# Performance work log

Measured on AMD Instinct MI355X. Metric: run time of the kernel, lower is better.

The kernel has to match this reference:

```python
import jax, jax.numpy as jnp
import numpy as np

B, S1, S2, H1, H2, HID = 8, 512, 512, 128, 128, 128

def setup_inputs() -> dict:
    key = jax.random.key(0)
    ks = jax.random.split(key, 8)
    return {
        "query": jax.random.normal(ks[0], (B, S1, H1), jnp.float32),
        "key": jax.random.normal(ks[1], (B, S2, H2), jnp.float32),
        "value": jax.random.normal(ks[2], (B, S2, H2), jnp.float32),
        "q_mask": jax.random.randint(ks[3], (B, S1), 0, 2, jnp.int32),
        "k_mask": jax.random.randint(ks[4], (B, S2), 0, 2, jnp.int32),
        # init_weights: Linear weight ~ N(0, 0.01), bias = 0
        "W1": jax.random.normal(ks[5], (HID, H1 + H2), jnp.float32) * 0.01,
        "b1": jnp.zeros((HID,), jnp.float32),
        "W2": jax.random.normal(ks[6], (1, HID), jnp.float32) * 0.01,
        "b2": jnp.zeros((1,), jnp.float32),
    }

def reference(query, key, value, q_mask, k_mask, W1, b1, W2, b2):
    h1 = query.shape[-1]
    # Linear on concat([q,k]) == q @ W1[:, :h1].T + k @ W1[:, h1:].T + b1
    qp = jnp.einsum('bsd,hd->bsh', query, W1[:, :h1]) + b1   # [B,S1,HID]
    kp = jnp.einsum('btd,hd->bth', key, W1[:, h1:])          # [B,S2,HID]
    h = jax.nn.relu(qp[:, :, None, :] + kp[:, None, :, :])   # [B,S1,S2,HID]
    s = jnp.einsum('bsth,h->bst', h, W2[0]) + b2[0]          # [B,S1,S2]
    mask = (q_mask[:, :, None] * k_mask[:, None, :]) > 0     # [B,S1,S2]
    A = jnp.where(mask, jnp.exp(s), 0.0)                     # masked_fill(-inf).exp()
    A_sum = jnp.clip(jnp.sum(A, axis=-1, keepdims=True), 2e-15, None)
    attn = A / A_sum
    return jnp.einsum('bst,btd->bsd', attn, value)           # [B,S1,H2]
```

## Files before the change

### kernel.cpp

```cpp
#include <hip/hip_runtime.h>

#define S 512
#define H 128
#define NROW 4096
#define TI 8

__global__ __launch_bounds__(256) void proj_kernel(
    const float* __restrict__ query, const float* __restrict__ key,
    const float* __restrict__ W1, const float* __restrict__ b1,
    float* __restrict__ qp, float* __restrict__ kp)
{
  __shared__ float w1t[128][130];
  const int bid = blockIdx.x;
  const bool isq = bid < 128;
  const float* __restrict__ src = isq ? query : key;
  const int rbase = (isq ? bid : bid - 128) * 32;
  const int off = isq ? 0 : 128;
  const int tid = threadIdx.x;

  for (int idx = tid; idx < 128 * 32; idx += 256) {
    const int d4 = idx & 31, h = idx >> 5;
    const float4 v = *(const float4*)(W1 + h * 256 + off + d4 * 4);
    w1t[d4 * 4 + 0][h] = v.x;
    w1t[d4 * 4 + 1][h] = v.y;
    w1t[d4 * 4 + 2][h] = v.z;
    w1t[d4 * 4 + 3][h] = v.w;
  }
  __syncthreads();

  const int w = __builtin_amdgcn_readfirstlane(tid >> 6);
  const int lane = tid & 63;
  const int r0 = rbase + w * 8;

  float acc[8][2];
  float2 bv = make_float2(0.f, 0.f);
  if (isq) bv = *(const float2*)(b1 + 2 * lane);
  #pragma unroll
  for (int r = 0; r < 8; r++) { acc[r][0] = bv.x; acc[r][1] = bv.y; }

  for (int dc = 0; dc < 128; dc += 8) {
    float qs[8][8];
    #pragma unroll
    for (int r = 0; r < 8; r++) {
      const float* sp = src + (size_t)(r0 + r) * H + dc;
      #pragma unroll
      for (int u = 0; u < 8; u++) qs[r][u] = sp[u];
    }
    #pragma unroll
    for (int dd = 0; dd < 8; dd++) {
      const float2 wv = *(const float2*)&w1t[dc + dd][2 * lane];
      #pragma unroll
      for (int r = 0; r < 8; r++) {
        acc[r][0] = __builtin_fmaf(qs[r][dd], wv.x, acc[r][0]);
        acc[r][1] = __builtin_fmaf(qs[r][dd], wv.y, acc[r][1]);
      }
    }
  }
  float* __restrict__ dst = isq ? qp : kp;
  #pragma unroll
  for (int r = 0; r < 8; r++) {
    *(float2*)(dst + (size_t)(r0 + r) * H + 2 * lane) =
        make_float2(acc[r][0], acc[r][1]);
  }
}

__global__ __launch_bounds__(256) void attn_kernel(
    const float* __restrict__ qp, const float* __restrict__ kp,
    const float* __restrict__ value, const int* __restrict__ q_mask,
    const int* __restrict__ k_mask, const float* __restrict__ W2,
    const float* __restrict__ b2,
    float* __restrict__ nump, float* __restrict__ denp)
{
  __shared__ float aT[4][64][12];
  __shared__ float numk[TI][132];
  __shared__ float denk[TI];

  const int it = blockIdx.x;
  const int jh = blockIdx.y;
  const int r0 = it * TI;
  const int b  = r0 >> 9;
  const int tid = threadIdx.x;
  const int w = __builtin_amdgcn_readfirstlane(tid >> 6);
  const int lane = tid & 63;
  const int jl = (jh << 8) + (w << 6) + lane;
  const int jg = (b << 9) + jl;
  const int km = k_mask[jg];
  const float* __restrict__ kprow = kp + (size_t)jg * H;
  const float b2v = b2[0];

  float s[TI];
  #pragma unroll
  for (int i = 0; i < TI; i++) s[i] = 0.f;

  for (int hc = 0; hc < H; hc += 16) {
    float kr[16];
    #pragma unroll
    for (int u = 0; u < 4; u++) {
      const float4 v4 = *(const float4*)(kprow + hc + u * 4);
      kr[u*4+0] = v4.x; kr[u*4+1] = v4.y; kr[u*4+2] = v4.z; kr[u*4+3] = v4.w;
    }
    float w2r[16];
    #pragma unroll
    for (int u = 0; u < 16; u++) w2r[u] = W2[hc + u];
    #pragma unroll
    for (int i = 0; i < TI; i++) {
      const float* __restrict__ qrow = qp + (size_t)(r0 + i) * H + hc;
      #pragma unroll
      for (int u = 0; u < 16; u++) {
        float t = fmaxf(qrow[u] + kr[u], 0.f);
        s[i] = __builtin_fmaf(t, w2r[u], s[i]);
      }
    }
  }

  float a[TI], den[TI];
  #pragma unroll
  for (int i = 0; i < TI; i++) {
    const int qm = q_mask[r0 + i];
    a[i] = (km > 0 && qm > 0) ? __expf(s[i] + b2v) : 0.f;
  }
  #pragma unroll
  for (int i = 0; i < TI; i++) {
    float d = a[i];
    #pragma unroll
    for (int m = 32; m >= 1; m >>= 1) d += __shfl_xor(d, m, 64);
    den[i] = d;
  }
  #pragma unroll
  for (int i = 0; i < TI; i++) aT[w][lane][i] = a[i];
  __syncthreads();

  const int lj = lane >> 5, lh = lane & 31;
  float nr[TI][4];
  #pragma unroll
  for (int i = 0; i < TI; i++) { nr[i][0]=0.f; nr[i][1]=0.f; nr[i][2]=0.f; nr[i][3]=0.f; }
  const float* __restrict__ vbase =
      value + ((size_t)b * S + (jh << 8) + (w << 6)) * H;

  for (int js = 0; js < 32; js++) {
    const int j = js * 2 + lj;
    const float4 vv = *(const float4*)(vbase + (size_t)j * H + lh * 4);
    float av[TI];
    { const float4 t0 = *(const float4*)&aT[w][j][0];
      const float4 t1 = *(const float4*)&aT[w][j][4];
      av[0]=t0.x; av[1]=t0.y; av[2]=t0.z; av[3]=t0.w;
      av[4]=t1.x; av[5]=t1.y; av[6]=t1.z; av[7]=t1.w; }
    #pragma unroll
    for (int i = 0; i < TI; i++) {
      nr[i][0] = __builtin_fmaf(av[i], vv.x, nr[i][0]);
      nr[i][1] = __builtin_fmaf(av[i], vv.y, nr[i][1]);
      nr[i][2] = __builtin_fmaf(av[i], vv.z, nr[i][2]);
      nr[i][3] = __builtin_fmaf(av[i], vv.w, nr[i][3]);
    }
  }
  #pragma unroll
  for (int i = 0; i < TI; i++) {
    #pragma unroll
    for (int k = 0; k < 4; k++) nr[i][k] += __shfl_xor(nr[i][k], 32, 64);
  }

  for (int r = 0; r < 4; r++) {
    if (w == r) {
      if (lj == 0) {
        #pragma unroll
        for (int i = 0; i < TI; i++) {
          float4* p = (float4*)&numk[i][lh * 4];
          if (r == 0) {
            *p = make_float4(nr[i][0], nr[i][1], nr[i][2], nr[i][3]);
          } else {
            float4 t = *p;
            t.x += nr[i][0]; t.y += nr[i][1]; t.z += nr[i][2]; t.w += nr[i][3];
            *p = t;
          }
        }
      }
      if (lane == 0) {
        #pragma unroll
        for (int i = 0; i < TI; i++)
          denk[i] = (r == 0) ? den[i] : denk[i] + den[i];
      }
    }
    __syncthreads();
  }

  {
    const int i = tid >> 5, seg = tid & 31;
    const float4 v = *(const float4*)&numk[i][seg * 4];
    float* dst = nump + ((size_t)jh * NROW + (size_t)(r0 + i)) * H + seg * 4;
    *(float4*)dst = v;
    if (tid < TI) denp[jh * NROW + r0 + tid] = denk[tid];
  }
}

__global__ __launch_bounds__(256) void finalize_kernel(
    const float* __restrict__ nump, const float* __restrict__ denp,
    float* __restrict__ out)
{
  const int idx = blockIdx.x * 256 + threadIdx.x;
  const int row = idx >> 5;
  const float4 a = *(const float4*)(nump + (size_t)idx * 4);
  const float4 c = *(const float4*)(nump + (size_t)NROW * H + (size_t)idx * 4);
  const float d = denp[row] + denp[NROW + row];
  const float inv = 1.f / fmaxf(d, 2e-15f);
  float4 o;
  o.x = (a.x + c.x) * inv; o.y = (a.y + c.y) * inv;
  o.z = (a.z + c.z) * inv; o.w = (a.w + c.w) * inv;
  *(float4*)(out + (size_t)idx * 4) = o;
}

extern "C" void kernel_launch(void* const* d_in, const int* in_sizes, int n_in,
                              void* d_out, int out_size, void* d_ws, size_t ws_size,
                              hipStream_t stream)
{
  (void)in_sizes; (void)n_in; (void)out_size; (void)ws_size;
  const float* query  = (const float*)d_in[0];
  const float* key    = (const float*)d_in[1];
  const float* value  = (const float*)d_in[2];
  const int*   q_mask = (const int*)d_in[3];
  const int*   k_mask = (const int*)d_in[4];
  const float* W1     = (const float*)d_in[5];
  const float* b1     = (const float*)d_in[6];
  const float* W2     = (const float*)d_in[7];
  const float* b2     = (const float*)d_in[8];
  float* out = (float*)d_out;

  float* ws   = (float*)d_ws;
  float* qp   = ws;
  float* kp   = ws + (size_t)NROW * H;
  float* nump = ws + (size_t)2 * NROW * H;
  float* denp = ws + (size_t)4 * NROW * H;

  proj_kernel<<<256, 256, 0, stream>>>(query, key, W1, b1, qp, kp);
  attn_kernel<<<dim3(512, 2), 256, 0, stream>>>(qp, kp, value, q_mask, k_mask,
                                                W2, b2, nump, denp);
  finalize_kernel<<<512, 256, 0, stream>>>(nump, denp, out);
}
```

Measured before the change: 121.7 us.

## Rewrite relu as abs identity and transpose key projection for coalesced loads

Uses relu(x) = (x + |x|)/2 so the linear part of the score splits into per-row terms (qp·W2/2, kp·W2/2). These terms are precomputed in the projection kernel, leaving an fma on fabs in the inner loop. The key projection is written transposed so adjacent lanes read adjacent addresses, and query rows plus a halved W2 are staged in shared memory instead of being reread from global memory. Projection blocks are halved in size so twice as many are launched. The costs are an extra shuffle reduction, a shared-memory transpose in the projection kernel, and slightly different floating-point rounding.

Result: slower. 127.4 us (+4.8%).

```diff
diff --git a/kernel.cpp b/kernel.cpp
--- a/kernel.cpp
+++ b/kernel.cpp
@@ -8,13 +8,16 @@
 __global__ __launch_bounds__(256) void proj_kernel(
     const float* __restrict__ query, const float* __restrict__ key,
     const float* __restrict__ W1, const float* __restrict__ b1,
-    float* __restrict__ qp, float* __restrict__ kp)
+    const float* __restrict__ W2,
+    float* __restrict__ qp, float* __restrict__ kpT,
+    float* __restrict__ qw, float* __restrict__ kw)
 {
   __shared__ float w1t[128][130];
+  __shared__ float kt[16][132];
   const int bid = blockIdx.x;
-  const bool isq = bid < 128;
+  const bool isq = bid < 256;
   const float* __restrict__ src = isq ? query : key;
-  const int rbase = (isq ? bid : bid - 128) * 32;
+  const int rbase = (isq ? bid : bid - 256) * 16;
   const int off = isq ? 0 : 128;
   const int tid = threadIdx.x;
 
@@ -30,19 +33,19 @@
 
   const int w = __builtin_amdgcn_readfirstlane(tid >> 6);
   const int lane = tid & 63;
-  const int r0 = rbase + w * 8;
-
-  float acc[8][2];
+  const int r0w = rbase + w * 4;
+
+  float acc[4][2];
   float2 bv = make_float2(0.f, 0.f);
   if (isq) bv = *(const float2*)(b1 + 2 * lane);
   #pragma unroll
-  for (int r = 0; r < 8; r++) { acc[r][0] = bv.x; acc[r][1] = bv.y; }
+  for (int r = 0; r < 4; r++) { acc[r][0] = bv.x; acc[r][1] = bv.y; }
 
   for (int dc = 0; dc < 128; dc += 8) {
-    float qs[8][8];
-    #pragma unroll
-    for (int r = 0; r < 8; r++) {
-      const float* sp = src + (size_t)(r0 + r) * H + dc;
+    float qs[4][8];
+    #pragma unroll
+    for (int r = 0; r < 4; r++) {
+      const float* sp = src + (size_t)(r0w + r) * H + dc;
       #pragma unroll
       for (int u = 0; u < 8; u++) qs[r][u] = sp[u];
     }
@@ -50,27 +53,57 @@
     for (int dd = 0; dd < 8; dd++) {
       const float2 wv = *(const float2*)&w1t[dc + dd][2 * lane];
       #pragma unroll
-      for (int r = 0; r < 8; r++) {
+      for (int r = 0; r < 4; r++) {
         acc[r][0] = __builtin_fmaf(qs[r][dd], wv.x, acc[r][0]);
         acc[r][1] = __builtin_fmaf(qs[r][dd], wv.y, acc[r][1]);
       }
     }
   }
-  float* __restrict__ dst = isq ? qp : kp;
-  #pragma unroll
-  for (int r = 0; r < 8; r++) {
-    *(float2*)(dst + (size_t)(r0 + r) * H + 2 * lane) =
-        make_float2(acc[r][0], acc[r][1]);
+
+  const float2 w2p = *(const float2*)(W2 + 2 * lane);
+  #pragma unroll
+  for (int r = 0; r < 4; r++) {
+    float t = acc[r][0] * w2p.x + acc[r][1] * w2p.y;
+    #pragma unroll
+    for (int m = 1; m <= 32; m <<= 1) t += __shfl_xor(t, m, 64);
+    if (lane == 0) {
+      float* dw = isq ? qw : kw;
+      dw[r0w + r] = 0.5f * t;
+    }
+  }
+
+  if (isq) {
+    #pragma unroll
+    for (int r = 0; r < 4; r++)
+      *(float2*)(qp + (size_t)(r0w + r) * H + 2 * lane) =
+          make_float2(acc[r][0], acc[r][1]);
+  } else {
+    #pragma unroll
+    for (int r = 0; r < 4; r++)
+      *(float2*)&kt[w * 4 + r][2 * lane] =
+          make_float2(acc[r][0], acc[r][1]);
+    __syncthreads();
+    const int h = tid >> 1, seg = tid & 1;
+    float tmp[8];
+    #pragma unroll
+    for (int c = 0; c < 8; c++) tmp[c] = kt[seg * 8 + c][h];
+    float* dst = kpT + (size_t)h * NROW + rbase + seg * 8;
+    *(float4*)dst = make_float4(tmp[0], tmp[1], tmp[2], tmp[3]);
+    *(float4*)(dst + 4) = make_float4(tmp[4], tmp[5], tmp[6], tmp[7]);
   }
 }
 
 __global__ __launch_bounds__(256) void attn_kernel(
-    const float* __restrict__ qp, const float* __restrict__ kp,
+    const float* __restrict__ qp, const float* __restrict__ kpT,
+    const float* __restrict__ qw, const float* __restrict__ kw,
     const float* __restrict__ value, const int* __restrict__ q_mask,
     const int* __restrict__ k_mask, const float* __restrict__ W2,
     const float* __restrict__ b2,
     float* __restrict__ nump, float* __restrict__ denp)
 {
+  __shared__ float qs[TI][128];
+  __shared__ float w2s[128];
+  __shared__ float qws[TI];
   __shared__ float aT[4][64][12];
   __shared__ float numk[TI][132];
   __shared__ float denk[TI];
@@ -85,30 +118,48 @@
   const int jl = (jh << 8) + (w << 6) + lane;
   const int jg = (b << 9) + jl;
   const int km = k_mask[jg];
-  const float* __restrict__ kprow = kp + (size_t)jg * H;
+  const float kwj = kw[jg];
   const float b2v = b2[0];
 
+  {
+    const int i = tid >> 5, c = tid & 31;
+    *(float4*)&qs[i][c * 4] = *(const float4*)(qp + (size_t)(r0 + i) * H + c * 4);
+    if (tid < 32) {
+      float4 t = *(const float4*)(W2 + tid * 4);
+      t.x *= 0.5f; t.y *= 0.5f; t.z *= 0.5f; t.w *= 0.5f;
+      *(float4*)&w2s[tid * 4] = t;
+    }
+    if (tid < TI) qws[tid] = qw[r0 + tid];
+  }
+  __syncthreads();
+
   float s[TI];
   #pragma unroll
   for (int i = 0; i < TI; i++) s[i] = 0.f;
+  const float* __restrict__ kcol = kpT + jg;
 
   for (int hc = 0; hc < H; hc += 16) {
     float kr[16];
     #pragma unroll
+    for (int u = 0; u < 16; u++) kr[u] = kcol[(hc + u) * NROW];
+    float w2c[16];
+    #pragma unroll
     for (int u = 0; u < 4; u++) {
-      const float4 v4 = *(const float4*)(kprow + hc + u * 4);
-      kr[u*4+0] = v4.x; kr[u*4+1] = v4.y; kr[u*4+2] = v4.z; kr[u*4+3] = v4.w;
-    }
-    float w2r[16];
-    #pragma unroll
-    for (int u = 0; u < 16; u++) w2r[u] = W2[hc + u];
+      const float4 t = *(const float4*)&w2s[hc + u * 4];
+      w2c[u*4+0] = t.x; w2c[u*4+1] = t.y; w2c[u*4+2] = t.z; w2c[u*4+3] = t.w;
+    }
     #pragma unroll
     for (int i = 0; i < TI; i++) {
-      const float* __restrict__ qrow = qp + (size_t)(r0 + i) * H + hc;
+      float qv[16];
+      #pragma unroll
+      for (int u = 0; u < 4; u++) {
+        const float4 t = *(const float4*)&qs[i][hc + u * 4];
+        qv[u*4+0] = t.x; qv[u*4+1] = t.y; qv[u*4+2] = t.z; qv[u*4+3] = t.w;
+      }
       #pragma unroll
       for (int u = 0; u < 16; u++) {
-        float t = fmaxf(qrow[u] + kr[u], 0.f);
-        s[i] = __builtin_fmaf(t, w2r[u], s[i]);
+        const float t = qv[u] + kr[u];
+        s[i] = __builtin_fmaf(fabsf(t), w2c[u], s[i]);
       }
     }
   }
@@ -117,7 +168,8 @@
   #pragma unroll
   for (int i = 0; i < TI; i++) {
     const int qm = q_mask[r0 + i];
-    a[i] = (km > 0 && qm > 0) ? __expf(s[i] + b2v) : 0.f;
+    const float sf = s[i] + qws[i] + kwj;
+    a[i] = (km > 0 && qm > 0) ? __expf(sf + b2v) : 0.f;
   }
   #pragma unroll
   for (int i = 0; i < TI; i++) {
@@ -226,12 +278,14 @@
 
   float* ws   = (float*)d_ws;
   float* qp   = ws;
-  float* kp   = ws + (size_t)NROW * H;
-  float* nump = ws + (size_t)2 * NROW * H;
-  float* denp = ws + (size_t)4 * NROW * H;
-
-  proj_kernel<<<256, 256, 0, stream>>>(query, key, W1, b1, qp, kp);
-  attn_kernel<<<dim3(512, 2), 256, 0, stream>>>(qp, kp, value, q_mask, k_mask,
-                                                W2, b2, nump, denp);
+  float* kpT  = ws + (size_t)NROW * H;
+  float* qw   = ws + (size_t)2 * NROW * H;
+  float* kw   = qw + NROW;
+  float* nump = kw + NROW;
+  float* denp = nump + (size_t)2 * NROW * H;
+
+  proj_kernel<<<512, 256, 0, stream>>>(query, key, W1, b1, W2, qp, kpT, qw, kw);
+  attn_kernel<<<dim3(512, 2), 256, 0, stream>>>(qp, kpT, qw, kw, value, q_mask,
+                                                k_mask, W2, b2, nump, denp);
   finalize_kernel<<<512, 256, 0, stream>>>(nump, denp, out);
 }
```

## Use relu(x)=(x+|x|)/2 split, fuse finalize into attention, transpose W1 once

Applied to the files above, without the earlier changes.

Rewrites relu(q+k)·w2 as 0.5·(q·w2 + k·w2) + 0.5·|q+k|·w2. The linear parts are precomputed per row in the projection kernel, which trims the inner loop to an add, an abs and an FMA. The attention kernel now covers all 512 keys per block with 512 threads and writes normalized output directly, so the split-K partial buffers and the finalize kernel are gone. W1 is transposed once by a small kernel and read from global memory instead of being re-transposed into LDS per block. kp is stored in an h-blocked layout for coalesced per-key loads. This adds a kernel launch and changes the reduction order.

Result: slower. 128.6 us (+5.7%).

```diff
diff --git a/kernel.cpp b/kernel.cpp
--- a/kernel.cpp
+++ b/kernel.cpp
@@ -5,207 +5,221 @@
 #define NROW 4096
 #define TI 8
 
+__global__ __launch_bounds__(256) void w1t_kernel(const float* __restrict__ W1,
+                                                  float* __restrict__ w1T) {
+  __shared__ float t[32][33];
+  const int d0 = (blockIdx.x & 7) * 32;
+  const int h0 = (blockIdx.x >> 3) * 32;
+  const int tx = threadIdx.x & 31, ty = threadIdx.x >> 5;
+  #pragma unroll
+  for (int r = 0; r < 4; r++)
+    t[ty + r * 8][tx] = W1[(h0 + ty + r * 8) * 256 + d0 + tx];
+  __syncthreads();
+  #pragma unroll
+  for (int r = 0; r < 4; r++)
+    w1T[(size_t)(d0 + ty + r * 8) * H + h0 + tx] = t[tx][ty + r * 8];
+}
+
 __global__ __launch_bounds__(256) void proj_kernel(
     const float* __restrict__ query, const float* __restrict__ key,
-    const float* __restrict__ W1, const float* __restrict__ b1,
-    float* __restrict__ qp, float* __restrict__ kp)
+    const float* __restrict__ w1T, const float* __restrict__ b1,
+    const float* __restrict__ W2, const float* __restrict__ b2,
+    float* __restrict__ qp, float* __restrict__ kp2,
+    float* __restrict__ qw, float* __restrict__ kw)
 {
-  __shared__ float w1t[128][130];
   const int bid = blockIdx.x;
-  const bool isq = bid < 128;
+  const bool isq = bid < 256;
   const float* __restrict__ src = isq ? query : key;
-  const int rbase = (isq ? bid : bid - 128) * 32;
-  const int off = isq ? 0 : 128;
+  const int rbase = (isq ? bid : bid - 256) * 16;
+  const int doff = isq ? 0 : 128;
   const int tid = threadIdx.x;
-
-  for (int idx = tid; idx < 128 * 32; idx += 256) {
-    const int d4 = idx & 31, h = idx >> 5;
-    const float4 v = *(const float4*)(W1 + h * 256 + off + d4 * 4);
-    w1t[d4 * 4 + 0][h] = v.x;
-    w1t[d4 * 4 + 1][h] = v.y;
-    w1t[d4 * 4 + 2][h] = v.z;
-    w1t[d4 * 4 + 3][h] = v.w;
-  }
-  __syncthreads();
-
   const int w = __builtin_amdgcn_readfirstlane(tid >> 6);
   const int lane = tid & 63;
-  const int r0 = rbase + w * 8;
-
-  float acc[8][2];
+  const int r0w = rbase + w * 4;
+
+  float acc[4][2];
   float2 bv = make_float2(0.f, 0.f);
   if (isq) bv = *(const float2*)(b1 + 2 * lane);
   #pragma unroll
-  for (int r = 0; r < 8; r++) { acc[r][0] = bv.x; acc[r][1] = bv.y; }
+  for (int r = 0; r < 4; r++) { acc[r][0] = bv.x; acc[r][1] = bv.y; }
 
   for (int dc = 0; dc < 128; dc += 8) {
-    float qs[8][8];
-    #pragma unroll
-    for (int r = 0; r < 8; r++) {
-      const float* sp = src + (size_t)(r0 + r) * H + dc;
+    float qs[4][8];
+    #pragma unroll
+    for (int r = 0; r < 4; r++) {
+      const float* sp = src + (size_t)(r0w + r) * H + dc;
       #pragma unroll
       for (int u = 0; u < 8; u++) qs[r][u] = sp[u];
     }
     #pragma unroll
     for (int dd = 0; dd < 8; dd++) {
-      const float2 wv = *(const float2*)&w1t[dc + dd][2 * lane];
+      const float2 wv =
+          *(const float2*)(w1T + (size_t)(doff + dc + dd) * H + 2 * lane);
       #pragma unroll
-      for (int r = 0; r < 8; r++) {
+      for (int r = 0; r < 4; r++) {
         acc[r][0] = __builtin_fmaf(qs[r][dd], wv.x, acc[r][0]);
         acc[r][1] = __builtin_fmaf(qs[r][dd], wv.y, acc[r][1]);
       }
     }
   }
-  float* __restrict__ dst = isq ? qp : kp;
-  #pragma unroll
-  for (int r = 0; r < 8; r++) {
-    *(float2*)(dst + (size_t)(r0 + r) * H + 2 * lane) =
-        make_float2(acc[r][0], acc[r][1]);
-  }
-}
-
-__global__ __launch_bounds__(256) void attn_kernel(
-    const float* __restrict__ qp, const float* __restrict__ kp,
+
+  const float2 w2p = *(const float2*)(W2 + 2 * lane);
+  const float b2v = b2[0];
+  #pragma unroll
+  for (int r = 0; r < 4; r++) {
+    float t = acc[r][0] * w2p.x + acc[r][1] * w2p.y;
+    #pragma unroll
+    for (int m = 1; m <= 32; m <<= 1) t += __shfl_xor(t, m, 64);
+    if (lane == 0) {
+      if (isq) qw[r0w + r] = 0.5f * t + b2v;
+      else     kw[r0w + r] = 0.5f * t;
+    }
+  }
+
+  if (isq) {
+    #pragma unroll
+    for (int r = 0; r < 4; r++)
+      *(float2*)(qp + (size_t)(r0w + r) * H + 2 * lane) =
+          make_float2(acc[r][0], acc[r][1]);
+  } else {
+    #pragma unroll
+    for (int r = 0; r < 4; r++)
+      *(float2*)(kp2 + ((size_t)(lane >> 3) * NROW + (r0w + r)) * 16 +
+                 (lane & 7) * 2) = make_float2(acc[r][0], acc[r][1]);
+  }
+}
+
+__global__ __launch_bounds__(512) void attn_kernel(
+    const float* __restrict__ qp, const float* __restrict__ kp2,
+    const float* __restrict__ qw, const float* __restrict__ kw,
     const float* __restrict__ value, const int* __restrict__ q_mask,
     const int* __restrict__ k_mask, const float* __restrict__ W2,
-    const float* __restrict__ b2,
-    float* __restrict__ nump, float* __restrict__ denp)
+    float* __restrict__ out)
 {
-  __shared__ float aT[4][64][12];
-  __shared__ float numk[TI][132];
-  __shared__ float denk[TI];
+  __shared__ float aT[8][64][8];
+  __shared__ float numw[8][TI][132];
+  __shared__ float denw[8][TI];
 
   const int it = blockIdx.x;
-  const int jh = blockIdx.y;
   const int r0 = it * TI;
   const int b  = r0 >> 9;
   const int tid = threadIdx.x;
   const int w = __builtin_amdgcn_readfirstlane(tid >> 6);
   const int lane = tid & 63;
-  const int jl = (jh << 8) + (w << 6) + lane;
-  const int jg = (b << 9) + jl;
+  const int jg = (b << 9) + (w << 6) + lane;
   const int km = k_mask[jg];
-  const float* __restrict__ kprow = kp + (size_t)jg * H;
-  const float b2v = b2[0];
+  const float kwj = kw[jg];
 
   float s[TI];
   #pragma unroll
   for (int i = 0; i < TI; i++) s[i] = 0.f;
 
-  for (int hc = 0; hc < H; hc += 16) {
-    float kr[16];
-    #pragma unroll
-    for (int u = 0; u < 4; u++) {
-      const float4 v4 = *(const float4*)(kprow + hc + u * 4);
-      kr[u*4+0] = v4.x; kr[u*4+1] = v4.y; kr[u*4+2] = v4.z; kr[u*4+3] = v4.w;
-    }
-    float w2r[16];
-    #pragma unroll
-    for (int u = 0; u < 16; u++) w2r[u] = W2[hc + u];
+  #pragma unroll
+  for (int hb = 0; hb < 8; hb++) {
+    const float* __restrict__ kptr = kp2 + (((size_t)hb * NROW + jg) << 4);
+    const float4 k0 = ((const float4*)kptr)[0];
+    const float4 k1 = ((const float4*)kptr)[1];
+    const float4 k2 = ((const float4*)kptr)[2];
+    const float4 k3 = ((const float4*)kptr)[3];
+    const float4* __restrict__ w2c = (const float4*)(W2 + hb * 16);
+    const float4 w0 = w2c[0], w1 = w2c[1], w2_ = w2c[2], w3 = w2c[3];
     #pragma unroll
     for (int i = 0; i < TI; i++) {
-      const float* __restrict__ qrow = qp + (size_t)(r0 + i) * H + hc;
-      #pragma unroll
-      for (int u = 0; u < 16; u++) {
-        float t = fmaxf(qrow[u] + kr[u], 0.f);
-        s[i] = __builtin_fmaf(t, w2r[u], s[i]);
-      }
-    }
-  }
-
-  float a[TI], den[TI];
+      const float4* __restrict__ qptr =
+          (const float4*)(qp + (size_t)(r0 + i) * H + hb * 16);
+      const float4 q0 = qptr[0], q1 = qptr[1], q2 = qptr[2], q3 = qptr[3];
+      float t, si = s[i];
+      t = q0.x + k0.x; si = __builtin_fmaf(fabsf(t), w0.x, si);
+      t = q0.y + k0.y; si = __builtin_fmaf(fabsf(t), w0.y, si);
+      t = q0.z + k0.z; si = __builtin_fmaf(fabsf(t), w0.z, si);
+      t = q0.w + k0.w; si = __builtin_fmaf(fabsf(t), w0.w, si);
+      t = q1.x + k1.x; si = __builtin_fmaf(fabsf(t), w1.x, si);
+      t = q1.y + k1.y; si = __builtin_fmaf(fabsf(t), w1.y, si);
+      t = q1.z + k1.z; si = __builtin_fmaf(fabsf(t), w1.z, si);
+      t = q1.w + k1.w; si = __builtin_fmaf(fabsf(t), w1.w, si);
+      t = q2.x + k2.x; si = __builtin_fmaf(fabsf(t), w2_.x, si);
+      t = q2.y + k2.y; si = __builtin_fmaf(fabsf(t), w2_.y, si);
+      t = q2.z + k2.z; si = __builtin_fmaf(fabsf(t), w2_.z, si);
+      t = q2.w + k2.w; si = __builtin_fmaf(fabsf(t), w2_.w, si);
+      t = q3.x + k3.x; si = __builtin_fmaf(fabsf(t), w3.x, si);
+      t = q3.y + k3.y; si = __builtin_fmaf(fabsf(t), w3.y, si);
+      t = q3.z + k3.z; si = __builtin_fmaf(fabsf(t), w3.z, si);
+      t = q3.w + k3.w; si = __builtin_fmaf(fabsf(t), w3.w, si);
+      s[i] = si;
+    }
+  }
+
+  float a[TI];
   #pragma unroll
   for (int i = 0; i < TI; i++) {
+    const float qws = qw[r0 + i];
     const int qm = q_mask[r0 + i];
-    a[i] = (km > 0 && qm > 0) ? __expf(s[i] + b2v) : 0.f;
-  }
-  #pragma unroll
-  for (int i = 0; i < TI; i++) {
-    float d = a[i];
-    #pragma unroll
-    for (int m = 32; m >= 1; m >>= 1) d += __shfl_xor(d, m, 64);
-    den[i] = d;
-  }
-  #pragma unroll
-  for (int i = 0; i < TI; i++) aT[w][lane][i] = a[i];
+    a[i] = (km > 0 && qm > 0) ? __expf(__builtin_fmaf(0.5f, s[i], qws + kwj))
+                              : 0.f;
+  }
+  #pragma unroll
+  for (int i = 0; i < TI; i += 2)
+    *(float2*)&aT[w][lane][i] = make_float2(a[i], a[i + 1]);
   __syncthreads();
 
   const int lj = lane >> 5, lh = lane & 31;
   float nr[TI][4];
-  #pragma unroll
-  for (int i = 0; i < TI; i++) { nr[i][0]=0.f; nr[i][1]=0.f; nr[i][2]=0.f; nr[i][3]=0.f; }
+  float dden[TI];
+  #pragma unroll
+  for (int i = 0; i < TI; i++) {
+    nr[i][0] = 0.f; nr[i][1] = 0.f; nr[i][2] = 0.f; nr[i][3] = 0.f;
+    dden[i] = 0.f;
+  }
   const float* __restrict__ vbase =
-      value + ((size_t)b * S + (jh << 8) + (w << 6)) * H;
+      value + ((size_t)b * S + (w << 6)) * H;
 
   for (int js = 0; js < 32; js++) {
     const int j = js * 2 + lj;
     const float4 vv = *(const float4*)(vbase + (size_t)j * H + lh * 4);
-    float av[TI];
-    { const float4 t0 = *(const float4*)&aT[w][j][0];
-      const float4 t1 = *(const float4*)&aT[w][j][4];
-      av[0]=t0.x; av[1]=t0.y; av[2]=t0.z; av[3]=t0.w;
-      av[4]=t1.x; av[5]=t1.y; av[6]=t1.z; av[7]=t1.w; }
+    const float4 a0 = *(const float4*)&aT[w][j][0];
+    const float4 a1 = *(const float4*)&aT[w][j][4];
+    const float av[8] = {a0.x, a0.y, a0.z, a0.w, a1.x, a1.y, a1.z, a1.w};
     #pragma unroll
     for (int i = 0; i < TI; i++) {
       nr[i][0] = __builtin_fmaf(av[i], vv.x, nr[i][0]);
       nr[i][1] = __builtin_fmaf(av[i], vv.y, nr[i][1]);
       nr[i][2] = __builtin_fmaf(av[i], vv.z, nr[i][2]);
       nr[i][3] = __builtin_fmaf(av[i], vv.w, nr[i][3]);
+      dden[i] += av[i];
     }
   }
   #pragma unroll
   for (int i = 0; i < TI; i++) {
     #pragma unroll
     for (int k = 0; k < 4; k++) nr[i][k] += __shfl_xor(nr[i][k], 32, 64);
-  }
-
-  for (int r = 0; r < 4; r++) {
-    if (w == r) {
-      if (lj == 0) {
-        #pragma unroll
-        for (int i = 0; i < TI; i++) {
-          float4* p = (float4*)&numk[i][lh * 4];
-          if (r == 0) {
-            *p = make_float4(nr[i][0], nr[i][1], nr[i][2], nr[i][3]);
-          } else {
-            float4 t = *p;
-            t.x += nr[i][0]; t.y += nr[i][1]; t.z += nr[i][2]; t.w += nr[i][3];
-            *p = t;
-          }
-        }
-      }
-      if (lane == 0) {
-        #pragma unroll
-        for (int i = 0; i < TI; i++)
-          denk[i] = (r == 0) ? den[i] : denk[i] + den[i];
-      }
-    }
-    __syncthreads();
-  }
+    dden[i] += __shfl_xor(dden[i], 32, 64);
+  }
+  if (lj == 0) {
+    #pragma unroll
+    for (int i = 0; i < TI; i++)
+      *(float4*)&numw[w][i][lh * 4] =
+          make_float4(nr[i][0], nr[i][1], nr[i][2], nr[i][3]);
+    if (lane == 0) {
+      #pragma unroll
+      for (int i = 0; i < TI; i++) denw[w][i] = dden[i];
+    }
+  }
+  __syncthreads();
 
   {
-    const int i = tid >> 5, seg = tid & 31;
-    const float4 v = *(const float4*)&numk[i][seg * 4];
-    float* dst = nump + ((size_t)jh * NROW + (size_t)(r0 + i)) * H + seg * 4;
-    *(float4*)dst = v;
-    if (tid < TI) denp[jh * NROW + r0 + tid] = denk[tid];
-  }
-}
-
-__global__ __launch_bounds__(256) void finalize_kernel(
-    const float* __restrict__ nump, const float* __restrict__ denp,
-    float* __restrict__ out)
-{
-  const int idx = blockIdx.x * 256 + threadIdx.x;
-  const int row = idx >> 5;
-  const float4 a = *(const float4*)(nump + (size_t)idx * 4);
-  const float4 c = *(const float4*)(nump + (size_t)NROW * H + (size_t)idx * 4);
-  const float d = denp[row] + denp[NROW + row];
-  const float inv = 1.f / fmaxf(d, 2e-15f);
-  float4 o;
-  o.x = (a.x + c.x) * inv; o.y = (a.y + c.y) * inv;
-  o.z = (a.z + c.z) * inv; o.w = (a.w + c.w) * inv;
-  *(float4*)(out + (size_t)idx * 4) = o;
+    const int i = w;
+    float2 acc = make_float2(0.f, 0.f);
+    float den = 0.f;
+    #pragma unroll
+    for (int ww = 0; ww < 8; ww++) {
+      const float2 p = *(const float2*)&numw[ww][i][lane * 2];
+      acc.x += p.x; acc.y += p.y;
+      den += denw[ww][i];
+    }
+    const float inv = 1.f / fmaxf(den, 2e-15f);
+    *(float2*)(out + (size_t)(r0 + i) * H + lane * 2) =
+        make_float2(acc.x * inv, acc.y * inv);
+  }
 }
 
 extern "C" void kernel_launch(void* const* d_in, const int* in_sizes, int n_in,
@@ -225,13 +239,15 @@
   float* out = (float*)d_out;
 
   float* ws   = (float*)d_ws;
-  float* qp   = ws;
-  float* kp   = ws + (size_t)NROW * H;
-  float* nump = ws + (size_t)2 * NROW * H;
-  float* denp = ws + (size_t)4 * NROW * H;
-
-  proj_kernel<<<256, 256, 0, stream>>>(query, key, W1, b1, qp, kp);
-  attn_kernel<<<dim3(512, 2), 256, 0, stream>>>(qp, kp, value, q_mask, k_mask,
-                                                W2, b2, nump, denp);
-  finalize_kernel<<<512, 256, 0, stream>>>(nump, denp, out);
-}
+  float* w1T  = ws;
+  float* qp   = w1T + 256 * H;
+  float* kp2  = qp + (size_t)NROW * H;
+  float* qw   = kp2 + (size_t)NROW * H;
+  float* kw   = qw + NROW;
+
+  w1t_kernel<<<32, 256, 0, stream>>>(W1, w1T);
+  proj_kernel<<<512, 256, 0, stream>>>(query, key, w1T, b1, W2, b2,
+                                       qp, kp2, qw, kw);
+  attn_kernel<<<512, 512, 0, stream>>>(qp, kp2, qw, kw, value, q_mask,
+                                       k_mask, W2, out);
+}
```
